# Kernel tuning notes

Measured on AMD Instinct MI355X. Metric: run time of the kernel, lower is better.

Reference implementation:

```python
import jax, jax.numpy as jnp
import numpy as np

B, L, D, H = 2, 2048, 2048, 16
HD = D // H          # head_dim = 128
LAT = HD // 4        # latent_dim = 32


def setup_inputs() -> dict:
    key = jax.random.key(0)
    ks = jax.random.split(key, 16)
    def w(k, shape, fan_in):
        return jax.random.normal(k, shape, jnp.float32) / np.float32(np.sqrt(fan_in))
    x = jax.random.normal(ks[0], (B, L, D), jnp.float32)
    # RoPE frequencies, stored as (cos, sin) pairs: [L, HD//2, 2]
    inv_freq = 1.0 / (10000.0 ** (np.arange(0, HD, 2, dtype=np.float32) / HD))
    ang = np.outer(np.arange(L, dtype=np.float32), inv_freq)
    freqs_cis = jnp.stack([jnp.asarray(np.cos(ang)), jnp.asarray(np.sin(ang))], axis=-1)
    return dict(
        x=x, freqs_cis=freqs_cis,
        Wq=w(ks[1], (D, D), D), bq=jnp.zeros((D,), jnp.float32),
        Wk=w(ks[2], (D, D), D), bk=jnp.zeros((D,), jnp.float32),
        Wv=w(ks[3], (D, D), D), bv=jnp.zeros((D,), jnp.float32),
        Wqc=w(ks[4], (LAT, HD), HD), bqc=jnp.zeros((LAT,), jnp.float32),
        Wkc=w(ks[5], (LAT, HD), HD), bkc=jnp.zeros((LAT,), jnp.float32),
        Wvc=w(ks[6], (LAT, HD), HD), bvc=jnp.zeros((LAT,), jnp.float32),
        Wd=w(ks[7], (HD, LAT), LAT), bd=jnp.zeros((HD,), jnp.float32),
        Wo=w(ks[8], (D, D), D), bo=jnp.zeros((D,), jnp.float32),
    )


def _rope(t, freqs_cis):
    # t: [B,H,L,HD]; freqs_cis: [L, HD//2, 2] (cos, sin)
    tp = t.reshape(t.shape[:-1] + (HD // 2, 2))
    a, b = tp[..., 0], tp[..., 1]
    cr = freqs_cis[:, :, 0]  # [L, HD//2]
    ci = freqs_cis[:, :, 1]
    ra = a * cr - b * ci
    rb = a * ci + b * cr
    return jnp.stack([ra, rb], axis=-1).reshape(t.shape)


def reference(x, freqs_cis, Wq, bq, Wk, bk, Wv, bv, Wqc, bqc, Wkc, bkc, Wvc, bvc, Wd, bd, Wo, bo):
    Bx, Lx, Dx = x.shape
    # QKV projections -> [B,H,L,HD]
    def proj(W, bias):
        return (x @ W.T + bias).reshape(Bx, Lx, H, HD).transpose(0, 2, 1, 3)
    q = proj(Wq, bq)
    k = proj(Wk, bk)
    v = proj(Wv, bv)
    q = _rope(q, freqs_cis)
    k = _rope(k, freqs_cis)
    # per-head compression to latent dim: [B,H,L,LAT]
    qc = q @ Wqc.T + bqc
    kc = k @ Wkc.T + bkc
    vc = v @ Wvc.T + bvc
    scores = jnp.einsum('bhie,bhje->bhij', qc, kc) / np.float32(np.sqrt(LAT))
    mask = jnp.triu(jnp.ones((Lx, Lx), bool), 1)  # future positions
    scores = jnp.where(mask, jnp.float32(-jnp.inf), scores)
    probs = jax.nn.softmax(scores, axis=-1)
    attn = jnp.einsum('bhij,bhje->bhie', probs, vc)  # [B,H,L,LAT]
    attn = attn @ Wd.T + bd                          # decompress -> [B,H,L,HD]
    attn = attn.transpose(0, 2, 1, 3).reshape(Bx, Lx, Dx)
    return attn @ Wo.T + bo
```

## Files before the change

### kernel.cpp

```cpp
#include <hip/hip_runtime.h>

typedef __attribute__((ext_vector_type(8))) __bf16 bf16x8;
typedef __attribute__((ext_vector_type(4))) __bf16 bf16x4;
typedef __attribute__((ext_vector_type(4))) float f32x4;
typedef __attribute__((ext_vector_type(16))) float f32x16;

#define LL 2048
#define DD 2048
#define HH 16
#define HDIM 128

__global__ __launch_bounds__(256)
void cvt_all(const float* __restrict__ x, const float* __restrict__ Wq,
             const float* __restrict__ Wk, const float* __restrict__ Wqc,
             const float* __restrict__ Wkc,
             __bf16* __restrict__ xb, __bf16* __restrict__ Wqb, __bf16* __restrict__ Wkb,
             __bf16* __restrict__ Wqcb, __bf16* __restrict__ Wkcb)
{
    size_t i = (size_t)blockIdx.x * 256 + threadIdx.x;
    const float* s; __bf16* d; size_t off;
    if (i < 2097152)      { s = x;   d = xb;   off = i; }
    else if (i < 3145728) { s = Wq;  d = Wqb;  off = i - 2097152; }
    else if (i < 4194304) { s = Wk;  d = Wkb;  off = i - 3145728; }
    else if (i < 4195328) { s = Wqc; d = Wqcb; off = i - 4194304; }
    else                  { s = Wkc; d = Wkcb; off = i - 4195328; }
    float4 v = *(const float4*)(s + off * 4);
    bf16x4 o = { (__bf16)v.x, (__bf16)v.y, (__bf16)v.z, (__bf16)v.w };
    *(bf16x4*)(d + off * 4) = o;
}

__global__ __launch_bounds__(256)
void build_wv_eff(const float* __restrict__ Wv, const float* __restrict__ Wvc,
                  const float* __restrict__ bv, const float* __restrict__ bvc,
                  __bf16* __restrict__ Wveff, float* __restrict__ bveff)
{
    __shared__ float WvcT[128][32];
    const int h = blockIdx.x, dc = blockIdx.y, tid = threadIdx.x;
    for (int i = tid; i < 4096; i += 256) WvcT[i & 127][i >> 7] = Wvc[i];
    __syncthreads();
    const int d  = dc * 64 + (tid & 63);
    const int o0 = (tid >> 6) * 8;
    float acc[8] = {};
    for (int j = 0; j < 128; ++j) {
        const float w = Wv[(size_t)(h * 128 + j) * 2048 + d];
        #pragma unroll
        for (int o = 0; o < 8; ++o) acc[o] += WvcT[j][o0 + o] * w;
    }
    #pragma unroll
    for (int o = 0; o < 8; ++o)
        Wveff[(size_t)(h * 32 + o0 + o) * 2048 + d] = (__bf16)acc[o];
    if (dc == 0 && tid < 32) {
        float s = bvc[tid];
        for (int j = 0; j < 128; ++j) s += WvcT[j][tid] * bv[h * 128 + j];
        bveff[h * 32 + tid] = s;
    }
}

__global__ __launch_bounds__(256)
void build_wo_eff(const float* __restrict__ Wo, const float* __restrict__ Wd,
                  __bf16* __restrict__ Woeff)
{
    __shared__ float WdL[128][32];
    const int dc = blockIdx.x, h = blockIdx.y, tid = threadIdx.x;
    for (int i = tid; i < 4096; i += 256) WdL[i >> 5][i & 31] = Wd[i];
    __syncthreads();
    const int dout = dc * 64 + (tid & 63);
    const int o0   = (tid >> 6) * 8;
    float acc[8] = {};
    const float* wrow = Wo + (size_t)dout * 2048 + h * 128;
    for (int u = 0; u < 128; ++u) {
        const float w = wrow[u];
        #pragma unroll
        for (int o = 0; o < 8; ++o) acc[o] += WdL[u][o0 + o] * w;
    }
    #pragma unroll
    for (int o = 0; o < 8; ++o)
        Woeff[(size_t)dout * 512 + h * 32 + o0 + o] = (__bf16)acc[o];
}

__global__ __launch_bounds__(256)
void build_bo_eff(const float* __restrict__ Wo, const float* __restrict__ bd,
                  const float* __restrict__ bo, float* __restrict__ boeff)
{
    __shared__ float bdL[128];
    const int tid = threadIdx.x;
    if (tid < 128) bdL[tid] = bd[tid];
    __syncthreads();
    const int d  = blockIdx.x * 32 + (tid >> 3);
    const int s0 = (tid & 7) * 64;
    float s = 0.f;
    const float* wrow = Wo + (size_t)d * 2048 + s0 * 4;
    for (int c4 = 0; c4 < 64; ++c4) {
        float4 wv = *(const float4*)(wrow + c4 * 4);
        const int cb = ((s0 + c4) * 4) & 127;
        s += wv.x * bdL[cb] + wv.y * bdL[cb + 1] + wv.z * bdL[cb + 2] + wv.w * bdL[cb + 3];
    }
    #pragma unroll
    for (int off = 4; off; off >>= 1) s += __shfl_down(s, off, 8);
    if ((tid & 7) == 0) boeff[d] = bo[d] + s;
}

typedef unsigned int u32;
typedef const __attribute__((address_space(1))) u32* gp_t;
typedef __attribute__((address_space(3))) u32* lp_t;
__device__ __forceinline__ void gload16(const __bf16* g, __bf16* l)
{
    __builtin_amdgcn_global_load_lds((gp_t)(const void*)g, (lp_t)(void*)l, 16, 0, 0);
}

#define MF16(a, b, c) __builtin_amdgcn_mfma_f32_16x16x32_bf16(a, b, c, 0, 0, 0)

__global__ __launch_bounds__(256, 3)
void gemm_qkv(const __bf16* __restrict__ A,
              const __bf16* __restrict__ Wq, const __bf16* __restrict__ Wk,
              const __bf16* __restrict__ Wveff,
              const float* __restrict__ bq, const float* __restrict__ bk,
              const float* __restrict__ bveff,
              const __bf16* __restrict__ Wqcb, const __bf16* __restrict__ Wkcb,
              const float* __restrict__ bqc, const float* __restrict__ bkc,
              const float* __restrict__ fc,
              __bf16* __restrict__ qc, __bf16* __restrict__ kc, __bf16* __restrict__ vt)
{
    __shared__ __bf16 lds[3][2][4096];

    const int bid = blockIdx.x;
    const int xcd = bid & 7;
    const int j   = bid >> 3;
    const int bx  = j >> 2;
    const int byl = j & 3;
    const int by  = xcd * 4 + byl;
    const int m0  = by * 128;
    const int which = (bx >= 32) ? 2 : (bx >> 4);
    const int n0  = (which == 2) ? (bx - 32) * 128 : (bx & 15) * 128;
    const __bf16* W = which == 0 ? Wq : which == 1 ? Wk : Wveff;

    const int tid  = threadIdx.x;
    const int wid  = tid >> 6;
    const int lane = tid & 63;
    const int wr   = wid >> 1;
    const int wc   = wid & 1;
    const int l15  = lane & 15;
    const int l4   = lane >> 4;
    const int swz  = (l4 ^ (l15 & 3) ^ ((l15 >> 2) & 3)) * 8;

    const int srl  = lane >> 2;
    const int scol = ((lane & 3) ^ (srl & 3) ^ ((srl >> 2) & 3)) * 8;
    const __bf16* gA0 = A + (size_t)(m0 + wid * 32 + srl) * 2048 + scol;
    const __bf16* gB0 = W + (size_t)(n0 + wid * 32 + srl) * 2048 + scol;

    #define STAGE(bb, kk)                                                \
    {   __bf16* dA = &lds[bb][0][wid * 1024];                            \
        __bf16* dB = &lds[bb][1][wid * 1024];                            \
        gload16(gA0 + (kk), dA);                                         \
        gload16(gA0 + (size_t)16 * 2048 + (kk), dA + 512);               \
        gload16(gB0 + (kk), dB);                                         \
        gload16(gB0 + (size_t)16 * 2048 + (kk), dB + 512);               \
    }
    #define RD_A(bb, mf) (*(const bf16x8*)&lds[bb][0][(wr * 64 + (mf) * 16 + l15) * 32 + swz])
    #define RD_B(bb, nf) (*(const bf16x8*)&lds[bb][1][(wc * 64 + (nf) * 16 + l15) * 32 + swz])

    f32x4 acc[4][4] = {};

    STAGE(0, 0) STAGE(1, 32)
    asm volatile("s_waitcnt vmcnt(4)" ::: "memory");
    __builtin_amdgcn_s_barrier();

    #define TB(RB, SB, VM, DOST, kk)                                          \
    {                                                                         \
        bf16x8 fa[4], fb[4];                                                  \
        fa[0] = RD_A(RB, 0); fa[1] = RD_A(RB, 1);                             \
        fa[2] = RD_A(RB, 2); fa[3] = RD_A(RB, 3);                             \
        fb[0] = RD_B(RB, 0); fb[1] = RD_B(RB, 1);                             \
        fb[2] = RD_B(RB, 2); fb[3] = RD_B(RB, 3);                             \
        if (DOST) STAGE(SB, kk)                                               \
        asm volatile("s_waitcnt lgkmcnt(0)" ::: "memory");                    \
        __builtin_amdgcn_sched_barrier(0);                                    \
        __builtin_amdgcn_s_setprio(1);                                        \
        _Pragma("unroll")                                                     \
        for (int mf = 0; mf < 4; ++mf)                                        \
            _Pragma("unroll")                                                 \
            for (int nf = 0; nf < 4; ++nf)                                    \
                acc[mf][nf] = MF16(fa[mf], fb[nf], acc[mf][nf]);              \
        __builtin_amdgcn_s_setprio(0);                                        \
        asm volatile("s_waitcnt vmcnt(" VM ")" ::: "memory");                 \
        __builtin_amdgcn_s_barrier();                                         \
    }

    for (int tt = 0; tt < 60; tt += 3) {
        const int kk = (tt + 2) * 32;
        TB(0, 2, "4", true, kk)
        TB(1, 0, "4", true, kk + 32)
        TB(2, 1, "4", true, kk + 64)
    }
    TB(0, 2, "4", true, 62 * 32)
    TB(1, 0, "4", true, 63 * 32)
    TB(2, 0, "0", false, 0)
    TB(0, 0, "0", false, 0)
    #undef TB
    #undef STAGE
    #undef RD_A
    #undef RD_B

    if (which < 2) {
        __bf16* qt = &lds[0][0][0];
        const float* bb = which ? bk : bq;
        #pragma unroll
        for (int nf = 0; nf < 4; ++nf) {
            const int col = wc * 64 + nf * 16 + l15;
            const float bv = bb[n0 + col];
            #pragma unroll
            for (int mf = 0; mf < 4; ++mf) {
                const int row0 = wr * 64 + mf * 16 + l4 * 4;
                #pragma unroll
                for (int rr = 0; rr < 4; ++rr)
                    qt[(row0 + rr) * 136 + col] = (__bf16)(acc[mf][nf][rr] + bv);
            }
        }
        __syncthreads();

        const int o   = lane & 31;
        const int hi  = lane >> 5;
        const int h   = bx & 15;
        const int b   = m0 >> 11;
        const int l0b = m0 & 2047;
        const int lrow = wid * 32 + o;
        const int l    = l0b + lrow;
        const __bf16* Wb = which ? Wkcb : Wqcb;
        const float*  bs = which ? bkc : bqc;
        const float* fcr = fc + (size_t)l * 128;

        bf16x8 wf[8];
        #pragma unroll
        for (int ks = 0; ks < 8; ++ks)
            wf[ks] = *(const bf16x8*)(Wb + o * 128 + ks * 16 + hi * 8);

        f32x16 C = {};
        #pragma unroll
        for (int ks = 0; ks < 8; ++ks) {
            bf16x8 af = *(const bf16x8*)&qt[lrow * 136 + ks * 16 + hi * 8];
            const float4 cA = *(const float4*)(fcr + (ks * 8 + hi * 4) * 2);
            const float4 cB = *(const float4*)(fcr + (ks * 8 + hi * 4) * 2 + 4);
            float a, b_;
            a = (float)af[0]; b_ = (float)af[1];
            af[0] = (__bf16)(a * cA.x - b_ * cA.y); af[1] = (__bf16)(a * cA.y + b_ * cA.x);
            a = (float)af[2]; b_ = (float)af[3];
            af[2] = (__bf16)(a * cA.z - b_ * cA.w); af[3] = (__bf16)(a * cA.w + b_ * cA.z);
            a = (float)af[4]; b_ = (float)af[5];
            af[4] = (__bf16)(a * cB.x - b_ * cB.y); af[5] = (__bf16)(a * cB.y + b_ * cB.x);
            a = (float)af[6]; b_ = (float)af[7];
            af[6] = (__bf16)(a * cB.z - b_ * cB.w); af[7] = (__bf16)(a * cB.w + b_ * cB.z);
            C = __builtin_amdgcn_mfma_f32_32x32x16_bf16(af, wf[ks], C, 0, 0, 0);
        }

        const float bias = bs[o];
        const float QSCALE = 0.17677669529663689f * 1.44269504088896340f;
        __bf16* outp = which ? kc : qc;
        const size_t g0row = (size_t)(b * 16 + h) * 2048 + l0b + wid * 32;
        #pragma unroll
        for (int r = 0; r < 16; ++r) {
            const int ro = (r & 3) + 8 * (r >> 2) + 4 * hi;
            float v = C[r] + bias;
            if (which == 0) v *= QSCALE;
            outp[(g0row + ro) * 32 + o] = (__bf16)v;
        }
    } else {
        #pragma unroll
        for (int nf = 0; nf < 4; ++nf) {
            const int ncol = n0 + wc * 64 + nf * 16 + l15;
            const float bv = bveff[ncol];
            const int hh = ncol >> 5, oo = ncol & 31;
            #pragma unroll
            for (int mf = 0; mf < 4; ++mf) {
                const int row0 = m0 + wr * 64 + mf * 16 + l4 * 4;
                const int b = row0 >> 11, l0 = row0 & 2047;
                bf16x4 pk = { (__bf16)(acc[mf][nf][0] + bv), (__bf16)(acc[mf][nf][1] + bv),
                              (__bf16)(acc[mf][nf][2] + bv), (__bf16)(acc[mf][nf][3] + bv) };
                *(bf16x4*)(vt + ((size_t)((b * 16 + hh) * 32 + oo)) * 2048 + l0) = pk;
            }
        }
    }
}

__global__ __launch_bounds__(256)
void gemm_ao(const __bf16* __restrict__ ao, const __bf16* __restrict__ Woeff,
             const float* __restrict__ boeff, float* __restrict__ out)
{
    __shared__ __bf16 As[128][64];
    __shared__ __bf16 Bs[128][64];
    const int bid = blockIdx.x;
    const int x   = bid & 7;
    const int jj  = bid >> 3;
    const int bx  = x * 2 + (jj & 1);
    const int by  = jj >> 1;
    const int m0  = by * 128;
    const int n0  = bx * 128;

    const int tid  = threadIdx.x;
    const int wave = tid >> 6;
    const int lane = tid & 63;
    const int wr   = (wave >> 1) * 64;
    const int wc   = (wave & 1) * 64;
    const int lr   = lane & 15;
    const int lk   = (lane >> 4) * 8;
    const int srow = wave * 32 + (lane >> 3);
    const int scol = (lane & 7) * 8;

    f32x4 acc[4][4] = {};
    __bf16* lA = &As[wave * 32][0];
    __bf16* lB = &Bs[wave * 32][0];
    const __bf16* Ww = Woeff + (size_t)(n0 + srow) * 512 + scol;

    for (int k0 = 0; k0 < 512; k0 += 64) {
        const int kk = k0 + scol;
        const int hblk = kk >> 5, oo = kk & 31;
        #pragma unroll
        for (int j = 0; j < 4; ++j) {
            const int r = m0 + srow + j * 8;
            const int b = r >> 11, l = r & 2047;
            gload16(ao + ((size_t)((b << 4) + hblk) * 2048 + l) * 32 + oo, lA + j * 512);
            gload16(Ww + (size_t)(j * 8) * 512 + k0, lB + j * 512);
        }
        __syncthreads();
        #pragma unroll
        for (int ks = 0; ks < 2; ++ks) {
            bf16x8 af[4], bfr[4];
            #pragma unroll
            for (int m = 0; m < 4; ++m)
                af[m] = *(const bf16x8*)(&As[wr + m * 16 + lr][ks * 32 + lk]);
            #pragma unroll
            for (int n = 0; n < 4; ++n)
                bfr[n] = *(const bf16x8*)(&Bs[wc + n * 16 + lr][ks * 32 + lk]);
            #pragma unroll
            for (int m = 0; m < 4; ++m)
                #pragma unroll
                for (int n = 0; n < 4; ++n)
                    acc[m][n] = MF16(af[m], bfr[n], acc[m][n]);
        }
        __syncthreads();
    }

    const int orow = (lane >> 4) * 4;
    #pragma unroll
    for (int n = 0; n < 4; ++n) {
        const int col = n0 + wc + n * 16 + lr;
        const float bv = boeff[col];
        #pragma unroll
        for (int m = 0; m < 4; ++m) {
            #pragma unroll
            for (int r = 0; r < 4; ++r) {
                const int row = m0 + wr + m * 16 + orow + r;
                out[(size_t)row * 2048 + col] = acc[m][n][r] + bv;
            }
        }
    }
}

__device__ __forceinline__ unsigned pkbf2(float a, float b)
{
    union { __bf16 h[2]; unsigned u; } x;
    x.h[0] = (__bf16)a; x.h[1] = (__bf16)b;
    return x.u;
}

#if __has_builtin(__builtin_amdgcn_permlane32_swap)
typedef unsigned int uint2v __attribute__((ext_vector_type(2)));
__device__ __forceinline__ void plswap(unsigned a, unsigned b, unsigned& w_lo, unsigned& w_hi, int)
{
    uint2v r = __builtin_amdgcn_permlane32_swap(a, b, false, false);
    w_lo = r[0]; w_hi = r[1];
}
#else
__device__ __forceinline__ void plswap(unsigned a, unsigned b, unsigned& w_lo, unsigned& w_hi, int hi)
{
    unsigned ax = (unsigned)__shfl_xor((int)a, 32);
    unsigned bx = (unsigned)__shfl_xor((int)b, 32);
    w_lo = hi ? bx : a;
    w_hi = hi ? b  : ax;
}
#endif

__global__ __launch_bounds__(64)
void attn_part(const __bf16* __restrict__ qc, const __bf16* __restrict__ kc,
               const __bf16* __restrict__ vt,
               float* __restrict__ pm, float* __restrict__ pl, float* __restrict__ po)
{
    const int id  = blockIdx.x;
    const int bhl = id & 7;
    const int c   = id >> 3;
    const int bhh = c / 160;
    const int lin = c - bhh * 160;
    int s, ci;
    if (lin < 16)      { s = lin; ci = 0; }
    else if (lin < 48) { int q = lin - 16; s = 16 + (q >> 1); ci = q & 1; }
    else if (lin < 96) { int q = lin - 48; int d = q / 3; s = 32 + d; ci = q - d * 3; }
    else               { int q = lin - 96; s = 48 + (q >> 2); ci = q & 3; }
    const int bh = bhh * 8 + bhl;

    const int lane = threadIdx.x;
    const int qcol = lane & 31;
    const int hi   = lane >> 5;

    const __bf16* qbase = qc + ((size_t)bh * LL + (size_t)s * 32) * 32;
    const __bf16* kbase = kc + (size_t)bh * LL * 32;
    const __bf16* vbase = vt + (size_t)bh * 32 * LL;

    const bf16x8 qf0 = *(const bf16x8*)(qbase + qcol * 32 + hi * 8);
    const bf16x8 qf1 = *(const bf16x8*)(qbase + qcol * 32 + 16 + hi * 8);

    float m = -1e30f, lsum = 0.f;
    f32x16 O = {};

    const int t0 = ci * 16;
    const int t1 = min(s, t0 + 15);

    const __bf16* krow = kbase + (size_t)(t0 * 32 + qcol) * 32 + hi * 8;
    const __bf16* vrow = vbase + (size_t)qcol * LL + t0 * 32 + hi * 8;
    bf16x8 kc0 = *(const bf16x8*)(krow);
    bf16x8 kc1 = *(const bf16x8*)(krow + 16);
    bf16x8 vc0 = *(const bf16x8*)(vrow);
    bf16x8 vc1 = *(const bf16x8*)(vrow + 16);

    for (int t = t0; t <= t1; ++t) {
        const int tn = (t < t1) ? t + 1 : t;
        const __bf16* krn = kbase + (size_t)(tn * 32 + qcol) * 32 + hi * 8;
        const __bf16* vrn = vbase + (size_t)qcol * LL + tn * 32 + hi * 8;
        bf16x8 kn0 = *(const bf16x8*)(krn);
        bf16x8 kn1 = *(const bf16x8*)(krn + 16);
        bf16x8 vn0 = *(const bf16x8*)(vrn);
        bf16x8 vn1 = *(const bf16x8*)(vrn + 16);

        f32x16 S = {};
        S = __builtin_amdgcn_mfma_f32_32x32x16_bf16(kc0, qf0, S, 0, 0, 0);
        S = __builtin_amdgcn_mfma_f32_32x32x16_bf16(kc1, qf1, S, 0, 0, 0);

        if (t == s) {
            #pragma unroll
            for (int r = 0; r < 16; ++r) {
                const int kl = (r & 3) + 8 * (r >> 2) + 4 * hi;
                if (kl > qcol) S[r] = -1e30f;
            }
        }
        float tm = S[0];
        #pragma unroll
        for (int r = 1; r < 16; ++r) tm = fmaxf(tm, S[r]);
        tm = fmaxf(tm, __shfl_xor(tm, 32));
        const float mn = fmaxf(m, tm);
        const float fr = exp2f(m - mn);
        m = mn;
        float p[16]; float ls = 0.f;
        #pragma unroll
        for (int r = 0; r < 16; ++r) { p[r] = exp2f(S[r] - m); ls += p[r]; }
        lsum = lsum * fr + ls;
        #pragma unroll
        for (int r = 0; r < 16; ++r) O[r] *= fr;

        unsigned w[8];
        #pragma unroll
        for (int i = 0; i < 8; ++i) w[i] = pkbf2(p[2 * i], p[2 * i + 1]);
        union PF { unsigned u[4]; bf16x8 v; } pf1, pf2;
        plswap(w[0], w[2], pf1.u[0], pf1.u[2], hi);
        plswap(w[1], w[3], pf1.u[1], pf1.u[3], hi);
        plswap(w[4], w[6], pf2.u[0], pf2.u[2], hi);
        plswap(w[5], w[7], pf2.u[1], pf2.u[3], hi);

        O = __builtin_amdgcn_mfma_f32_32x32x16_bf16(vc0, pf1.v, O, 0, 0, 0);
        O = __builtin_amdgcn_mfma_f32_32x32x16_bf16(vc1, pf2.v, O, 0, 0, 0);

        kc0 = kn0; kc1 = kn1; vc0 = vn0; vc1 = vn1;
    }

    const float L = lsum + __shfl_xor(lsum, 32);
    const size_t g = (size_t)bh * LL + (size_t)s * 32 + qcol;
    const size_t slot = g * 4 + ci;
    if (hi == 0) { pm[slot] = m; pl[slot] = L; }
    float* pp = po + slot * 32;
    #pragma unroll
    for (int g4 = 0; g4 < 4; ++g4) {
        float4 v = { O[g4 * 4 + 0], O[g4 * 4 + 1], O[g4 * 4 + 2], O[g4 * 4 + 3] };
        *(float4*)(pp + g4 * 8 + 4 * hi) = v;
    }
}

__global__ __launch_bounds__(256)
void attn_comb(const float* __restrict__ pm, const float* __restrict__ pl,
               const float* __restrict__ po, __bf16* __restrict__ ao)
{
    const int g = blockIdx.x * 256 + threadIdx.x;
    const int i = g & (LL - 1);
    const int nch = (i >> 9) + 1;
    float m = -1e30f;
    for (int c = 0; c < nch; ++c) m = fmaxf(m, pm[(size_t)g * 4 + c]);
    float L = 0.f;
    float o[32] = {};
    for (int c = 0; c < nch; ++c) {
        const float w = exp2f(pm[(size_t)g * 4 + c] - m);
        L += w * pl[(size_t)g * 4 + c];
        const float* pp = po + ((size_t)g * 4 + c) * 32;
        #pragma unroll
        for (int d4 = 0; d4 < 8; ++d4) {
            float4 v = *(const float4*)(pp + d4 * 4);
            o[d4*4+0] += w * v.x; o[d4*4+1] += w * v.y;
            o[d4*4+2] += w * v.z; o[d4*4+3] += w * v.w;
        }
    }
    const float inv = 1.f / L;
    #pragma unroll
    for (int d8 = 0; d8 < 4; ++d8) {
        bf16x8 v;
        #pragma unroll
        for (int j = 0; j < 8; ++j) v[j] = (__bf16)(o[d8 * 8 + j] * inv);
        *(bf16x8*)(ao + (size_t)g * 32 + d8 * 8) = v;
    }
}

extern "C" void kernel_launch(void* const* d_in, const int* in_sizes, int n_in,
                              void* d_out, int out_size, void* d_ws, size_t ws_size,
                              hipStream_t stream)
{
    const float* x   = (const float*)d_in[0];
    const float* fc  = (const float*)d_in[1];
    const float* Wq  = (const float*)d_in[2];
    const float* bq  = (const float*)d_in[3];
    const float* Wk  = (const float*)d_in[4];
    const float* bk  = (const float*)d_in[5];
    const float* Wv  = (const float*)d_in[6];
    const float* bv  = (const float*)d_in[7];
    const float* Wqc = (const float*)d_in[8];
    const float* bqc = (const float*)d_in[9];
    const float* Wkc = (const float*)d_in[10];
    const float* bkc = (const float*)d_in[11];
    const float* Wvc = (const float*)d_in[12];
    const float* bvc = (const float*)d_in[13];
    const float* Wd  = (const float*)d_in[14];
    const float* bd  = (const float*)d_in[15];
    const float* Wo  = (const float*)d_in[16];
    const float* bo  = (const float*)d_in[17];
    float* out = (float*)d_out;

    const size_t MB = 1048576;
    char* w = (char*)d_ws;
    __bf16* xb    = (__bf16*)(w);
    __bf16* Wqb   = (__bf16*)(w + 16 * MB);
    __bf16* Wkb   = (__bf16*)(w + 24 * MB);
    __bf16* Wveff = (__bf16*)(w + 32 * MB);
    __bf16* qcbf  = (__bf16*)(w + 66 * MB);
    __bf16* kcbf  = (__bf16*)(w + 70 * MB);
    __bf16* vtbf  = (__bf16*)(w + 74 * MB);
    __bf16* aobf  = (__bf16*)(w + 78 * MB);
    __bf16* Wqcb  = (__bf16*)(w + 82 * MB);
    __bf16* Wkcb  = (__bf16*)(w + 82 * MB + 8192);
    __bf16* Woeff = (__bf16*)(w + 83 * MB);
    float*  boeff = (float*)(w + 85 * MB);
    float*  bveff = (float*)(w + 85 * MB + 8192);

    float* po = (float*)d_ws;
    float* pm = (float*)(w + 32 * MB);
    float* pl = (float*)(w + 33 * MB);

    if (ws_size < (size_t)90 * MB) return;

    cvt_all<<<16392, 256, 0, stream>>>(x, Wq, Wk, Wqc, Wkc, xb, Wqb, Wkb, Wqcb, Wkcb);
    build_wv_eff<<<dim3(16, 32), 256, 0, stream>>>(Wv, Wvc, bv, bvc, Wveff, bveff);
    build_wo_eff<<<dim3(32, 16), 256, 0, stream>>>(Wo, Wd, Woeff);
    build_bo_eff<<<64, 256, 0, stream>>>(Wo, bd, bo, boeff);

    gemm_qkv<<<1152, 256, 0, stream>>>(xb, Wqb, Wkb, Wveff, bq, bk, bveff,
                                       Wqcb, Wkcb, bqc, bkc, fc, qcbf, kcbf, vtbf);

    attn_part<<<5120, 64, 0, stream>>>(qcbf, kcbf, vtbf, pm, pl, po);
    attn_comb<<<256, 256, 0, stream>>>(pm, pl, po, aobf);

    gemm_ao<<<512, 256, 0, stream>>>(aobf, Woeff, boeff, out);
}
```

Measured before the change: 225.6 us.

## Widen QKV GEMM tile to 128x256 and process two heads per block

The fused QKV projection GEMM tile grows from 128x128 to 128x256 along N, so each block computes 32 accumulator fragments per wave and the grid halves to 576 blocks. The RoPE and compression epilogue now loops over two heads, staging each half through LDS with extra barriers. This raises arithmetic intensity and cuts repeated loads of the A tile. In exchange it uses more registers and LDS, lowers the occupancy hint from 3 to 2, and reduces the number of blocks available to fill the GPU.

```diff
diff --git a/kernel.cpp b/kernel.cpp
--- a/kernel.cpp
+++ b/kernel.cpp
@@ -110,7 +110,7 @@
 
 #define MF16(a, b, c) __builtin_amdgcn_mfma_f32_16x16x32_bf16(a, b, c, 0, 0, 0)
 
-__global__ __launch_bounds__(256, 3)
+__global__ __launch_bounds__(256, 2)
 void gemm_qkv(const __bf16* __restrict__ A,
               const __bf16* __restrict__ Wq, const __bf16* __restrict__ Wk,
               const __bf16* __restrict__ Wveff,
@@ -121,7 +121,7 @@
               const float* __restrict__ fc,
               __bf16* __restrict__ qc, __bf16* __restrict__ kc, __bf16* __restrict__ vt)
 {
-    __shared__ __bf16 lds[3][2][4096];
+    __shared__ __bf16 lds[3][12288];
 
     const int bid = blockIdx.x;
     const int xcd = bid & 7;
@@ -130,8 +130,8 @@
     const int byl = j & 3;
     const int by  = xcd * 4 + byl;
     const int m0  = by * 128;
-    const int which = (bx >= 32) ? 2 : (bx >> 4);
-    const int n0  = (which == 2) ? (bx - 32) * 128 : (bx & 15) * 128;
+    const int which = (bx >= 16) ? 2 : (bx >> 3);
+    const int n0  = (which == 2) ? (bx - 16) * 256 : (bx & 7) * 256;
     const __bf16* W = which == 0 ? Wq : which == 1 ? Wk : Wveff;
 
     const int tid  = threadIdx.x;
@@ -146,32 +146,36 @@
     const int srl  = lane >> 2;
     const int scol = ((lane & 3) ^ (srl & 3) ^ ((srl >> 2) & 3)) * 8;
     const __bf16* gA0 = A + (size_t)(m0 + wid * 32 + srl) * 2048 + scol;
-    const __bf16* gB0 = W + (size_t)(n0 + wid * 32 + srl) * 2048 + scol;
+    const __bf16* gB0 = W + (size_t)(n0 + wid * 64 + srl) * 2048 + scol;
 
     #define STAGE(bb, kk)                                                \
-    {   __bf16* dA = &lds[bb][0][wid * 1024];                            \
-        __bf16* dB = &lds[bb][1][wid * 1024];                            \
+    {   __bf16* dA = &lds[bb][wid * 1024];                               \
+        __bf16* dB = &lds[bb][4096 + wid * 2048];                        \
         gload16(gA0 + (kk), dA);                                         \
         gload16(gA0 + (size_t)16 * 2048 + (kk), dA + 512);               \
         gload16(gB0 + (kk), dB);                                         \
         gload16(gB0 + (size_t)16 * 2048 + (kk), dB + 512);               \
-    }
-    #define RD_A(bb, mf) (*(const bf16x8*)&lds[bb][0][(wr * 64 + (mf) * 16 + l15) * 32 + swz])
-    #define RD_B(bb, nf) (*(const bf16x8*)&lds[bb][1][(wc * 64 + (nf) * 16 + l15) * 32 + swz])
-
-    f32x4 acc[4][4] = {};
+        gload16(gB0 + (size_t)32 * 2048 + (kk), dB + 1024);              \
+        gload16(gB0 + (size_t)48 * 2048 + (kk), dB + 1536);              \
+    }
+    #define RD_A(bb, mf) (*(const bf16x8*)&lds[bb][(wr * 64 + (mf) * 16 + l15) * 32 + swz])
+    #define RD_B(bb, nf) (*(const bf16x8*)&lds[bb][4096 + (wc * 128 + (nf) * 16 + l15) * 32 + swz])
+
+    f32x4 acc[4][8] = {};
 
     STAGE(0, 0) STAGE(1, 32)
-    asm volatile("s_waitcnt vmcnt(4)" ::: "memory");
+    asm volatile("s_waitcnt vmcnt(6)" ::: "memory");
     __builtin_amdgcn_s_barrier();
 
     #define TB(RB, SB, VM, DOST, kk)                                          \
     {                                                                         \
-        bf16x8 fa[4], fb[4];                                                  \
+        bf16x8 fa[4], fb[8];                                                  \
         fa[0] = RD_A(RB, 0); fa[1] = RD_A(RB, 1);                             \
         fa[2] = RD_A(RB, 2); fa[3] = RD_A(RB, 3);                             \
         fb[0] = RD_B(RB, 0); fb[1] = RD_B(RB, 1);                             \
         fb[2] = RD_B(RB, 2); fb[3] = RD_B(RB, 3);                             \
+        fb[4] = RD_B(RB, 4); fb[5] = RD_B(RB, 5);                             \
+        fb[6] = RD_B(RB, 6); fb[7] = RD_B(RB, 7);                             \
         if (DOST) STAGE(SB, kk)                                               \
         asm volatile("s_waitcnt lgkmcnt(0)" ::: "memory");                    \
         __builtin_amdgcn_sched_barrier(0);                                    \
@@ -179,7 +183,7 @@
         _Pragma("unroll")                                                     \
         for (int mf = 0; mf < 4; ++mf)                                        \
             _Pragma("unroll")                                                 \
-            for (int nf = 0; nf < 4; ++nf)                                    \
+            for (int nf = 0; nf < 8; ++nf)                                    \
                 acc[mf][nf] = MF16(fa[mf], fb[nf], acc[mf][nf]);              \
         __builtin_amdgcn_s_setprio(0);                                        \
         asm volatile("s_waitcnt vmcnt(" VM ")" ::: "memory");                 \
@@ -188,12 +192,12 @@
 
     for (int tt = 0; tt < 60; tt += 3) {
         const int kk = (tt + 2) * 32;
-        TB(0, 2, "4", true, kk)
-        TB(1, 0, "4", true, kk + 32)
-        TB(2, 1, "4", true, kk + 64)
-    }
-    TB(0, 2, "4", true, 62 * 32)
-    TB(1, 0, "4", true, 63 * 32)
+        TB(0, 2, "6", true, kk)
+        TB(1, 0, "6", true, kk + 32)
+        TB(2, 1, "6", true, kk + 64)
+    }
+    TB(0, 2, "6", true, 62 * 32)
+    TB(1, 0, "6", true, 63 * 32)
     TB(2, 0, "0", false, 0)
     TB(0, 0, "0", false, 0)
     #undef TB
@@ -202,71 +206,77 @@
     #undef RD_B
 
     if (which < 2) {
-        __bf16* qt = &lds[0][0][0];
-        const float* bb = which ? bk : bq;
-        #pragma unroll
-        for (int nf = 0; nf < 4; ++nf) {
-            const int col = wc * 64 + nf * 16 + l15;
-            const float bv = bb[n0 + col];
-            #pragma unroll
-            for (int mf = 0; mf < 4; ++mf) {
-                const int row0 = wr * 64 + mf * 16 + l4 * 4;
-                #pragma unroll
-                for (int rr = 0; rr < 4; ++rr)
-                    qt[(row0 + rr) * 136 + col] = (__bf16)(acc[mf][nf][rr] + bv);
-            }
-        }
-        __syncthreads();
-
+        __bf16* qt = &lds[0][0];
+        const float* bb_ = which ? bk : bq;
+        const __bf16* Wb = which ? Wkcb : Wqcb;
+        const float*  bs = which ? bkc : bqc;
         const int o   = lane & 31;
         const int hi  = lane >> 5;
-        const int h   = bx & 15;
         const int b   = m0 >> 11;
         const int l0b = m0 & 2047;
         const int lrow = wid * 32 + o;
         const int l    = l0b + lrow;
-        const __bf16* Wb = which ? Wkcb : Wqcb;
-        const float*  bs = which ? bkc : bqc;
         const float* fcr = fc + (size_t)l * 128;
+        const float QSCALE = 0.17677669529663689f * 1.44269504088896340f;
+        __bf16* outp = which ? kc : qc;
 
         bf16x8 wf[8];
         #pragma unroll
         for (int ks = 0; ks < 8; ++ks)
             wf[ks] = *(const bf16x8*)(Wb + o * 128 + ks * 16 + hi * 8);
 
-        f32x16 C = {};
-        #pragma unroll
-        for (int ks = 0; ks < 8; ++ks) {
-            bf16x8 af = *(const bf16x8*)&qt[lrow * 136 + ks * 16 + hi * 8];
-            const float4 cA = *(const float4*)(fcr + (ks * 8 + hi * 4) * 2);
-            const float4 cB = *(const float4*)(fcr + (ks * 8 + hi * 4) * 2 + 4);
-            float a, b_;
-            a = (float)af[0]; b_ = (float)af[1];
-            af[0] = (__bf16)(a * cA.x - b_ * cA.y); af[1] = (__bf16)(a * cA.y + b_ * cA.x);
-            a = (float)af[2]; b_ = (float)af[3];
-            af[2] = (__bf16)(a * cA.z - b_ * cA.w); af[3] = (__bf16)(a * cA.w + b_ * cA.z);
-            a = (float)af[4]; b_ = (float)af[5];
-            af[4] = (__bf16)(a * cB.x - b_ * cB.y); af[5] = (__bf16)(a * cB.y + b_ * cB.x);
-            a = (float)af[6]; b_ = (float)af[7];
-            af[6] = (__bf16)(a * cB.z - b_ * cB.w); af[7] = (__bf16)(a * cB.w + b_ * cB.z);
-            C = __builtin_amdgcn_mfma_f32_32x32x16_bf16(af, wf[ks], C, 0, 0, 0);
-        }
-
-        const float bias = bs[o];
-        const float QSCALE = 0.17677669529663689f * 1.44269504088896340f;
-        __bf16* outp = which ? kc : qc;
-        const size_t g0row = (size_t)(b * 16 + h) * 2048 + l0b + wid * 32;
-        #pragma unroll
-        for (int r = 0; r < 16; ++r) {
-            const int ro = (r & 3) + 8 * (r >> 2) + 4 * hi;
-            float v = C[r] + bias;
-            if (which == 0) v *= QSCALE;
-            outp[(g0row + ro) * 32 + o] = (__bf16)v;
+        #pragma unroll
+        for (int half = 0; half < 2; ++half) {
+            if (wc == half) {
+                #pragma unroll
+                for (int nf = 0; nf < 8; ++nf) {
+                    const int col = nf * 16 + l15;
+                    const float bv = bb_[n0 + half * 128 + col];
+                    #pragma unroll
+                    for (int mf = 0; mf < 4; ++mf) {
+                        const int row0 = wr * 64 + mf * 16 + l4 * 4;
+                        #pragma unroll
+                        for (int rr = 0; rr < 4; ++rr)
+                            qt[(row0 + rr) * 136 + col] = (__bf16)(acc[mf][nf][rr] + bv);
+                    }
+                }
+            }
+            __syncthreads();
+
+            const int h = (n0 >> 7) + half;
+            f32x16 C = {};
+            #pragma unroll
+            for (int ks = 0; ks < 8; ++ks) {
+                bf16x8 af = *(const bf16x8*)&qt[lrow * 136 + ks * 16 + hi * 8];
+                const float4 cA = *(const float4*)(fcr + (ks * 8 + hi * 4) * 2);
+                const float4 cB = *(const float4*)(fcr + (ks * 8 + hi * 4) * 2 + 4);
+                float a, b_;
+                a = (float)af[0]; b_ = (float)af[1];
+                af[0] = (__bf16)(a * cA.x - b_ * cA.y); af[1] = (__bf16)(a * cA.y + b_ * cA.x);
+                a = (float)af[2]; b_ = (float)af[3];
+                af[2] = (__bf16)(a * cA.z - b_ * cA.w); af[3] = (__bf16)(a * cA.w + b_ * cA.z);
+                a = (float)af[4]; b_ = (float)af[5];
+                af[4] = (__bf16)(a * cB.x - b_ * cB.y); af[5] = (__bf16)(a * cB.y + b_ * cB.x);
+                a = (float)af[6]; b_ = (float)af[7];
+                af[6] = (__bf16)(a * cB.z - b_ * cB.w); af[7] = (__bf16)(a * cB.w + b_ * cB.z);
+                C = __builtin_amdgcn_mfma_f32_32x32x16_bf16(af, wf[ks], C, 0, 0, 0);
+            }
+
+            const float bias = bs[o];
+            const size_t g0row = (size_t)(b * 16 + h) * 2048 + l0b + wid * 32;
+            #pragma unroll
+            for (int r = 0; r < 16; ++r) {
+                const int ro = (r & 3) + 8 * (r >> 2) + 4 * hi;
+                float v = C[r] + bias;
+                if (which == 0) v *= QSCALE;
+                outp[(g0row + ro) * 32 + o] = (__bf16)v;
+            }
+            __syncthreads();
         }
     } else {
         #pragma unroll
-        for (int nf = 0; nf < 4; ++nf) {
-            const int ncol = n0 + wc * 64 + nf * 16 + l15;
+        for (int nf = 0; nf < 8; ++nf) {
+            const int ncol = n0 + wc * 128 + nf * 16 + l15;
             const float bv = bveff[ncol];
             const int hh = ncol >> 5, oo = ncol & 31;
             #pragma unroll
@@ -564,8 +574,8 @@
     build_wo_eff<<<dim3(32, 16), 256, 0, stream>>>(Wo, Wd, Woeff);
     build_bo_eff<<<64, 256, 0, stream>>>(Wo, bd, bo, boeff);
 
-    gemm_qkv<<<1152, 256, 0, stream>>>(xb, Wqb, Wkb, Wveff, bq, bk, bveff,
-                                       Wqcb, Wkcb, bqc, bkc, fc, qcbf, kcbf, vtbf);
+    gemm_qkv<<<576, 256, 0, stream>>>(xb, Wqb, Wkb, Wveff, bq, bk, bveff,
+                                      Wqcb, Wkcb, bqc, bkc, fc, qcbf, kcbf, vtbf);
 
     attn_part<<<5120, 64, 0, stream>>>(qcbf, kcbf, vtbf, pm, pl, po);
     attn_comb<<<256, 256, 0, stream>>>(pm, pl, po, aobf);
```

Result: no change. 229.4 us (+1.7%).
